# Optimization experiments

Hardware: AMD Instinct MI355X
Metric: run time of the kernel (lower is better)

Reference implementation:

```python
import jax, jax.numpy as jnp
import numpy as np

V, D, H, L, S = 50257, 1024, 16, 4, 4096
DH = D // H  # 64
DF = 4 * D   # 4096


def _layernorm(x, g, b, eps=1e-5):
    m = jnp.mean(x, axis=-1, keepdims=True)
    v = jnp.mean(jnp.square(x - m), axis=-1, keepdims=True)
    return (x - m) / jnp.sqrt(v + eps) * g + b


def _pos_encoding(s, d):
    # standard sinusoidal positional encoding [s, d]
    pos = jnp.arange(s, dtype=jnp.float32)[:, None]
    i = jnp.arange(d // 2, dtype=jnp.float32)[None, :]
    ang = pos * jnp.exp(-(2.0 * i / d) * jnp.log(10000.0))
    return jnp.concatenate([jnp.sin(ang), jnp.cos(ang)], axis=-1)


def setup_inputs() -> dict:
    key = jax.random.key(0)
    ks = jax.random.split(key, 8)
    s = 0.02
    return {
        "tokens": jax.random.randint(ks[0], (S,), 0, V),
        "emb": jax.random.normal(ks[1], (V, D), jnp.float32) * s,
        "Wq": jax.random.normal(ks[2], (L, H, D, DH), jnp.float32) * s,
        "bq": jnp.zeros((L, H, DH), jnp.float32),
        "Wk": jax.random.normal(ks[3], (L, H, D, DH), jnp.float32) * s,
        "bk": jnp.zeros((L, H, DH), jnp.float32),
        "Wv": jax.random.normal(ks[4], (L, H, D, DH), jnp.float32) * s,
        "bv": jnp.zeros((L, H, DH), jnp.float32),
        "ln1_g": jnp.ones((L, D), jnp.float32),
        "ln1_b": jnp.zeros((L, D), jnp.float32),
        "W1": jax.random.normal(ks[5], (L, D, DF), jnp.float32) * s,
        "b1": jnp.zeros((L, DF), jnp.float32),
        "W2": jax.random.normal(ks[6], (L, DF, D), jnp.float32) * s,
        "b2": jnp.zeros((L, D), jnp.float32),
        "ln2_g": jnp.ones((L, D), jnp.float32),
        "ln2_b": jnp.zeros((L, D), jnp.float32),
        "Wout": jax.random.normal(ks[7], (D, V), jnp.float32) * s,
        "bout": jnp.zeros((V,), jnp.float32),
    }


def reference(tokens, emb, Wq, bq, Wk, bk, Wv, bv, ln1_g, ln1_b,
              W1, b1, W2, b2, ln2_g, ln2_b, Wout, bout):
    x = emb[tokens] + _pos_encoding(S, D)          # [S, D]
    scale = 1.0 / jnp.sqrt(jnp.float32(DH))
    for l in range(L):
        # per-head projections: [H, S, DH]
        q = jnp.einsum("sd,hde->hse", x, Wq[l]) + bq[l][:, None, :]
        k = jnp.einsum("sd,hde->hse", x, Wk[l]) + bk[l][:, None, :]
        v = jnp.einsum("sd,hde->hse", x, Wv[l]) + bv[l][:, None, :]
        att = jax.nn.softmax(jnp.einsum("hse,hte->hst", q, k) * scale, axis=-1)
        y = jnp.einsum("hst,hte->hse", att, v)      # [H, S, DH]
        y = jnp.transpose(y, (1, 0, 2)).reshape(S, D)  # concat heads
        x = _layernorm(x + y, ln1_g[l], ln1_b[l])
        y = jnp.maximum(x @ W1[l] + b1[l], 0.0) @ W2[l] + b2[l]  # FFN
        x = _layernorm(x + y, ln2_g[l], ln2_b[l])
    logits = x @ Wout + bout                        # [S, V]
    return jax.nn.softmax(logits, axis=-1)
```

## Files before the change

kernel.cpp:

```cpp
#include <hip/hip_runtime.h>
#include <math.h>

#define S_LEN  4096
#define DMODEL 1024
#define NHEAD  16
#define DHEAD  64
#define DFF    4096
#define NLAYER 4
#define VOCAB  50257
#define NCBP   400

typedef unsigned short ushort_t;
typedef __attribute__((ext_vector_type(8))) __bf16 bf16x8;
typedef __attribute__((ext_vector_type(4))) float f32x4;

static __device__ __forceinline__ ushort_t f2bf(float f) {
  union { float f; unsigned u; } x; x.f = f;
  unsigned r = x.u + 0x7fffu + ((x.u >> 16) & 1u);
  return (ushort_t)(r >> 16);
}
static __device__ __forceinline__ float bf2f(ushort_t h) {
  union { unsigned u; float f; } x; x.u = ((unsigned)h) << 16;
  return x.f;
}
static __device__ __forceinline__ float exp2fast(float x) {
  return __builtin_amdgcn_exp2f(x);
}

#define GLOAD_LDS16(gp, lp) \
  __builtin_amdgcn_global_load_lds((const __attribute__((address_space(1))) void*)(gp), \
                                   (__attribute__((address_space(3))) void*)(lp), 16, 0, 0)

#define QSCALE 0.18033688011112042f

__global__ __launch_bounds__(256) void embed_kernel(
    const int* __restrict__ tokens, const float* __restrict__ emb,
    float* __restrict__ x, ushort_t* __restrict__ xh)
{
  int s = blockIdx.x;
  int tok = tokens[s];
  int d0 = threadIdx.x * 4;
  const double lf = 0.01798894603901598653;
  float4 ev = *(const float4*)(emb + (size_t)tok * DMODEL + d0);
  float o[4]; float evr[4] = {ev.x, ev.y, ev.z, ev.w};
  #pragma unroll
  for (int j = 0; j < 4; ++j) {
    int d = d0 + j;
    int i = (d < 512) ? d : d - 512;
    double ang = (double)s * exp(-lf * (double)i);
    float pe = (d < 512) ? (float)sin(ang) : (float)cos(ang);
    o[j] = evr[j] + pe;
  }
  *(float4*)(x + (size_t)s * DMODEL + d0) = make_float4(o[0], o[1], o[2], o[3]);
  ushort_t hv[4];
  #pragma unroll
  for (int j = 0; j < 4; ++j) hv[j] = f2bf(o[j]);
  *(ushort4*)(xh + (size_t)s * DMODEL + d0) = make_ushort4(hv[0], hv[1], hv[2], hv[3]);
}

__global__ __launch_bounds__(256)
void transpose_split(const float* __restrict__ in, ushort_t* __restrict__ oh,
                     ushort_t* __restrict__ ol,
                     long in_zstr, long out_zoff, long in_z2str, long out_z2off,
                     int zdiv, int in_rstride, int Kout, int Nvalid)
{
  __shared__ float tile[64][65];
  int z1 = blockIdx.z % zdiv, z2 = blockIdx.z / zdiv;
  long ioff = (long)z1 * in_zstr + (long)z2 * in_z2str;
  long ooff = (long)z1 * out_zoff + (long)z2 * out_z2off;
  const float* inz = in + ioff;
  ushort_t* ohz = oh + ooff;
  ushort_t* olz = ol + ooff;
  int k0 = blockIdx.x * 64, n0 = blockIdx.y * 64;
  int t = threadIdx.x;
  #pragma unroll
  for (int i = 0; i < 4; ++i) {
    int idx = t + i * 256;
    int kk = idx >> 4, c4 = idx & 15;
    #pragma unroll
    for (int j = 0; j < 4; ++j) {
      int n = n0 + c4 * 4 + j;
      float v = (n < Nvalid) ? inz[(long)(k0 + kk) * in_rstride + n] : 0.f;
      tile[c4 * 4 + j][kk] = v;
    }
  }
  __syncthreads();
  #pragma unroll
  for (int i = 0; i < 4; ++i) {
    int idx = t + i * 256;
    int nn = idx >> 4, k4 = idx & 15;
    ushort_t hv[4], lv[4];
    #pragma unroll
    for (int j = 0; j < 4; ++j) {
      float v = tile[nn][k4 * 4 + j];
      hv[j] = f2bf(v);
      lv[j] = f2bf(v - bf2f(hv[j]));
    }
    long ob = (long)(n0 + nn) * Kout + k0 + k4 * 4;
    *(ushort4*)(ohz + ob) = make_ushort4(hv[0], hv[1], hv[2], hv[3]);
    *(ushort4*)(olz + ob) = make_ushort4(lv[0], lv[1], lv[2], lv[3]);
  }
}

__global__ __launch_bounds__(256)
void transpose_h(const float* __restrict__ in, ushort_t* __restrict__ oh,
                 int in_rstride, int Kout, int Nvalid)
{
  __shared__ float tile[64][65];
  int k0 = blockIdx.x * 64, n0 = blockIdx.y * 64;
  int t = threadIdx.x;
  #pragma unroll
  for (int i = 0; i < 4; ++i) {
    int idx = t + i * 256;
    int kk = idx >> 4, c4 = idx & 15;
    #pragma unroll
    for (int j = 0; j < 4; ++j) {
      int n = n0 + c4 * 4 + j;
      float v = (n < Nvalid) ? in[(long)(k0 + kk) * in_rstride + n] : 0.f;
      tile[c4 * 4 + j][kk] = v;
    }
  }
  __syncthreads();
  #pragma unroll
  for (int i = 0; i < 4; ++i) {
    int idx = t + i * 256;
    int nn = idx >> 4, k4 = idx & 15;
    ushort_t hv[4];
    #pragma unroll
    for (int j = 0; j < 4; ++j) hv[j] = f2bf(tile[nn][k4 * 4 + j]);
    long ob = (long)(n0 + nn) * Kout + k0 + k4 * 4;
    *(ushort4*)(oh + ob) = make_ushort4(hv[0], hv[1], hv[2], hv[3]);
  }
}

__global__ __launch_bounds__(256)
void concat3_kernel(const float* __restrict__ a, const float* __restrict__ b,
                    const float* __restrict__ c, float* __restrict__ o,
                    int n, long lstrA, long lstrO)
{
  int i = blockIdx.x * 256 + threadIdx.x;
  long l = blockIdx.y;
  if (i < n) {
    o[l * lstrO + i]         = a[l * lstrA + i];
    o[l * lstrO + n + i]     = b[l * lstrA + i];
    o[l * lstrO + 2 * n + i] = c[l * lstrA + i];
  }
}

template<int EPI, bool RELU>
__global__ __launch_bounds__(512, 2)
void gemm8p(const ushort_t* __restrict__ Ah,
            const ushort_t* __restrict__ Bh, const ushort_t* __restrict__ Bl,
            const float* __restrict__ bias, float* __restrict__ C,
            ushort_t* __restrict__ O0, ushort_t* __restrict__ O1,
            ushort_t* __restrict__ O2, ushort_t* __restrict__ O4,
            int K, int ldk, long ldc, long czStride)
{
  constexpr int BUFSTR = 3 * 8192;
  constexpr int OBH = 8192, OBL = 16384;
  __shared__ ushort_t lds[2 * BUFSTR];

  const int t = threadIdx.x;
  const int l = t & 63;
  const int w = t >> 6;
  const int wr = w >> 2;
  const int wc = w & 3;
  const int lrow = l & 15;
  const int lk = (l >> 4) * 8;
  const int l8 = l * 8;
  const long m0 = (long)blockIdx.x * 256;
  const long n0 = (long)blockIdx.y * 256;
  const long kz = (long)blockIdx.z * K;

  const ushort_t *agp[2], *bgp[2], *blgp[2];
  int dst[2];
  #pragma unroll
  for (int i = 0; i < 2; ++i) {
    int s = i * 8 + w;
    dst[i] = s * 512 + l8;
    agp[i]  = Ah + (m0 + s * 16 + lrow) * (long)ldk + kz + lk;
    bgp[i]  = Bh + (n0 + s * 16 + lrow) * (long)ldk + kz + lk;
    blgp[i] = Bl + (n0 + s * 16 + lrow) * (long)ldk + kz + lk;
  }

  f32x4 acc[8][4];
  #pragma unroll
  for (int m = 0; m < 8; ++m)
    #pragma unroll
    for (int n = 0; n < 4; ++n) acc[m][n] = (f32x4)0.f;

  GLOAD_LDS16(agp[0],  &lds[dst[0]]);
  GLOAD_LDS16(agp[1],  &lds[dst[1]]);
  GLOAD_LDS16(bgp[0],  &lds[OBH + dst[0]]);
  GLOAD_LDS16(bgp[1],  &lds[OBH + dst[1]]);
  GLOAD_LDS16(blgp[0], &lds[OBL + dst[0]]);
  GLOAD_LDS16(blgp[1], &lds[OBL + dst[1]]);

  const int nk = K >> 5;
  int cur = 0;
  for (int kt = 0; kt < nk; ++kt) {
    const int knx = (kt + 1 < nk) ? (kt + 1) * 32 : 0;
    ushort_t* cb = &lds[cur * BUFSTR];
    ushort_t* nb = &lds[(cur ^ 1) * BUFSTR];
    bf16x8 af[8], bhf[4], blf[4];

    asm volatile("s_waitcnt vmcnt(2)" ::: "memory");
    __builtin_amdgcn_sched_barrier(0);
    __builtin_amdgcn_s_barrier();
    __builtin_amdgcn_sched_barrier(0);
    #pragma unroll
    for (int m = 0; m < 8; ++m)
      af[m] = *(const bf16x8*)&cb[(wr * 8 + m) * 512 + l8];
    #pragma unroll
    for (int n = 0; n < 4; ++n)
      bhf[n] = *(const bf16x8*)&cb[OBH + (wc * 4 + n) * 512 + l8];
    GLOAD_LDS16(agp[0] + knx, &nb[dst[0]]);
    GLOAD_LDS16(agp[1] + knx, &nb[dst[1]]);
    GLOAD_LDS16(bgp[0] + knx, &nb[OBH + dst[0]]);
    __builtin_amdgcn_s_setprio(1);
    #pragma unroll
    for (int m = 0; m < 8; ++m)
      #pragma unroll
      for (int n = 0; n < 4; ++n)
        acc[m][n] = __builtin_amdgcn_mfma_f32_16x16x32_bf16(af[m], bhf[n], acc[m][n], 0, 0, 0);
    __builtin_amdgcn_s_setprio(0);
    __builtin_amdgcn_sched_barrier(0);

    asm volatile("s_waitcnt vmcnt(3)" ::: "memory");
    __builtin_amdgcn_sched_barrier(0);
    __builtin_amdgcn_s_barrier();
    __builtin_amdgcn_sched_barrier(0);
    #pragma unroll
    for (int n = 0; n < 4; ++n)
      blf[n] = *(const bf16x8*)&cb[OBL + (wc * 4 + n) * 512 + l8];
    GLOAD_LDS16(bgp[1] + knx,  &nb[OBH + dst[1]]);
    GLOAD_LDS16(blgp[0] + knx, &nb[OBL + dst[0]]);
    GLOAD_LDS16(blgp[1] + knx, &nb[OBL + dst[1]]);
    __builtin_amdgcn_s_setprio(1);
    #pragma unroll
    for (int m = 0; m < 8; ++m)
      #pragma unroll
      for (int n = 0; n < 4; ++n)
        acc[m][n] = __builtin_amdgcn_mfma_f32_16x16x32_bf16(af[m], blf[n], acc[m][n], 0, 0, 0);
    __builtin_amdgcn_s_setprio(0);
    __builtin_amdgcn_sched_barrier(0);
    cur ^= 1;
  }
  asm volatile("s_waitcnt vmcnt(0)" ::: "memory");

  if constexpr (EPI == 2) {
    #pragma unroll
    for (int n = 0; n < 4; ++n) {
      long col = n0 + wc * 64 + n * 16 + lrow;
      float bv = bias[col];
      #pragma unroll
      for (int m = 0; m < 8; ++m) {
        #pragma unroll
        for (int r = 0; r < 4; ++r) {
          long row = m0 + wr * 128 + m * 16 + (l >> 4) * 4 + r;
          float v = acc[m][n][r] + bv;
          int c = (int)col;
          if (c < 1024) {
            int hh = c >> 6, e = c & 63;
            float qv = v * QSCALE;
            ushort_t hi = f2bf(qv);
            size_t a = ((size_t)hh * S_LEN + row) * 64 + e;
            O0[a] = hi; O1[a] = f2bf(qv - bf2f(hi));
          } else if (c < 2048) {
            int cc = c - 1024;
            int hh = cc >> 6, e = cc & 63;
            size_t a = ((size_t)hh * S_LEN + row) * 64 + e;
            O2[a] = f2bf(v);
          } else {
            int cc = c - 2048;
            int hh = cc >> 6, e = cc & 63;
            size_t a = ((size_t)hh * DHEAD + e) * S_LEN + row;
            O4[a] = f2bf(v);
          }
        }
      }
    }
  } else if constexpr (EPI == 1) {
    long col4[4]; float bv4[4];
    #pragma unroll
    for (int n = 0; n < 4; ++n) {
      col4[n] = n0 + wc * 64 + n * 16 + lrow;
      bv4[n] = bias[col4[n]];
    }
    #pragma unroll
    for (int m = 0; m < 8; ++m) {
      #pragma unroll
      for (int r = 0; r < 4; ++r) {
        long row = m0 + wr * 128 + m * 16 + (l >> 4) * 4 + r;
        ushort_t* crow = O0 + row * ldc;
        #pragma unroll
        for (int n = 0; n < 4; ++n) {
          float v = acc[m][n][r] + bv4[n];
          if (RELU) v = fmaxf(v, 0.f);
          crow[col4[n]] = f2bf(v);
        }
      }
    }
  } else {
    float* Cz = C + (long)blockIdx.z * czStride;
    long col4[4];
    #pragma unroll
    for (int n = 0; n < 4; ++n) col4[n] = n0 + wc * 64 + n * 16 + lrow;
    #pragma unroll
    for (int m = 0; m < 8; ++m) {
      #pragma unroll
      for (int r = 0; r < 4; ++r) {
        long row = m0 + wr * 128 + m * 16 + (l >> 4) * 4 + r;
        float* crow = Cz + row * ldc;
        #pragma unroll
        for (int n = 0; n < 4; ++n) crow[col4[n]] = acc[m][n][r];
      }
    }
  }
}

template<bool BOUND>
__global__ __launch_bounds__(512, 2)
void gemm1p(const ushort_t* __restrict__ Ah, const ushort_t* __restrict__ Bh,
            const float* __restrict__ bias, float* __restrict__ C,
            int K, int ldk, long ldc, int Nlimit,
            float* __restrict__ Ppart, int cbbase)
{
  constexpr int OB = 8192;
  constexpr int BUFSTR = 16384;
  __shared__ ushort_t lds[3 * BUFSTR];
  __shared__ float psum[1024];

  const int t = threadIdx.x;
  const int l = t & 63;
  const int w = t >> 6;
  const int wr = w >> 2;
  const int wc = w & 3;
  const int lrow = l & 15;
  const int lk = (l >> 4) * 8;
  const int l8 = l * 8;
  const long m0 = (long)blockIdx.x * 256;
  const long n0 = (long)blockIdx.y * 256;

  const ushort_t *agp[2], *bgp[2];
  int dst[2];
  #pragma unroll
  for (int i = 0; i < 2; ++i) {
    int s = i * 8 + w;
    dst[i] = s * 512 + l8;
    agp[i] = Ah + (m0 + s * 16 + lrow) * (long)ldk + lk;
    bgp[i] = Bh + (n0 + s * 16 + lrow) * (long)ldk + lk;
  }

  f32x4 acc[8][4];
  #pragma unroll
  for (int m = 0; m < 8; ++m)
    #pragma unroll
    for (int n = 0; n < 4; ++n) acc[m][n] = (f32x4)0.f;

  GLOAD_LDS16(agp[0], &lds[dst[0]]);
  GLOAD_LDS16(agp[1], &lds[dst[1]]);
  GLOAD_LDS16(bgp[0], &lds[OB + dst[0]]);
  GLOAD_LDS16(bgp[1], &lds[OB + dst[1]]);
  GLOAD_LDS16(agp[0] + 32, &lds[BUFSTR + dst[0]]);
  GLOAD_LDS16(agp[1] + 32, &lds[BUFSTR + dst[1]]);
  GLOAD_LDS16(bgp[0] + 32, &lds[BUFSTR + OB + dst[0]]);
  GLOAD_LDS16(bgp[1] + 32, &lds[BUFSTR + OB + dst[1]]);

  const int nk = K >> 5;
  int cur = 0;
  for (int kt = 0; kt < nk; ++kt) {
    ushort_t* cb = &lds[cur * BUFSTR];
    int nxt = cur + 2; if (nxt >= 3) nxt -= 3;
    ushort_t* nb = &lds[nxt * BUFSTR];
    bf16x8 af[8], bhf[4];

    asm volatile("s_waitcnt vmcnt(4)" ::: "memory");
    __builtin_amdgcn_sched_barrier(0);
    __builtin_amdgcn_s_barrier();
    __builtin_amdgcn_sched_barrier(0);
    #pragma unroll
    for (int m = 0; m < 8; ++m)
      af[m] = *(const bf16x8*)&cb[(wr * 8 + m) * 512 + l8];
    #pragma unroll
    for (int n = 0; n < 4; ++n)
      bhf[n] = *(const bf16x8*)&cb[OB + (wc * 4 + n) * 512 + l8];
    const int knx2 = (kt + 2 < nk) ? (kt + 2) * 32 : 0;
    GLOAD_LDS16(agp[0] + knx2, &nb[dst[0]]);
    GLOAD_LDS16(agp[1] + knx2, &nb[dst[1]]);
    GLOAD_LDS16(bgp[0] + knx2, &nb[OB + dst[0]]);
    GLOAD_LDS16(bgp[1] + knx2, &nb[OB + dst[1]]);
    __builtin_amdgcn_s_setprio(1);
    #pragma unroll
    for (int m = 0; m < 8; ++m)
      #pragma unroll
      for (int n = 0; n < 4; ++n)
        acc[m][n] = __builtin_amdgcn_mfma_f32_16x16x32_bf16(af[m], bhf[n], acc[m][n], 0, 0, 0);
    __builtin_amdgcn_s_setprio(0);
    __builtin_amdgcn_sched_barrier(0);
    cur = (cur == 2) ? 0 : cur + 1;
  }
  asm volatile("s_waitcnt vmcnt(0)" ::: "memory");

  float smr[8][4];
  #pragma unroll
  for (int m = 0; m < 8; ++m)
    #pragma unroll
    for (int r = 0; r < 4; ++r) smr[m][r] = 0.f;
  long col4[4]; float bv4[4]; bool cok4[4];
  #pragma unroll
  for (int n = 0; n < 4; ++n) {
    col4[n] = n0 + wc * 64 + n * 16 + lrow;
    cok4[n] = (!BOUND) || (col4[n] < (long)Nlimit);
    bv4[n] = cok4[n] ? bias[col4[n]] : 0.f;
  }
  #pragma unroll
  for (int m = 0; m < 8; ++m) {
    #pragma unroll
    for (int r = 0; r < 4; ++r) {
      long row = m0 + wr * 128 + m * 16 + (l >> 4) * 4 + r;
      float* crow = C + row * ldc;
      #pragma unroll
      for (int n = 0; n < 4; ++n) {
        float e = cok4[n] ? __expf(acc[m][n][r] + bv4[n]) : 0.f;
        if (cok4[n]) crow[col4[n]] = e;
        smr[m][r] += e;
      }
    }
  }
  #pragma unroll
  for (int m = 0; m < 8; ++m) {
    #pragma unroll
    for (int r = 0; r < 4; ++r) {
      float s = smr[m][r];
      s += __shfl_xor(s, 1);
      s += __shfl_xor(s, 2);
      s += __shfl_xor(s, 4);
      s += __shfl_xor(s, 8);
      if (lrow == 0)
        psum[wc * 256 + wr * 128 + m * 16 + (l >> 4) * 4 + r] = s;
    }
  }
  __syncthreads();
  if (t < 256) {
    float s = psum[t] + psum[256 + t] + psum[512 + t] + psum[768 + t];
    Ppart[(m0 + t) * NCBP + cbbase + blockIdx.y] = s;
  }
}

__global__ __launch_bounds__(256)
void attn_mfma(const ushort_t* __restrict__ qh, const ushort_t* __restrict__ ql,
               const ushort_t* __restrict__ kh, const ushort_t* __restrict__ vt,
               float* __restrict__ y)
{
  __shared__ ushort_t lds[24576];

  const int t = threadIdx.x, l = t & 63, w = t >> 6;
  const int lrow = l & 15, lhi = l >> 4;
  const int h = blockIdx.y;
  const int bw = blockIdx.x * 128 + w * 32;
  const size_t hS = (size_t)h * S_LEN * DHEAD;
  const size_t hV = (size_t)h * DHEAD * S_LEN;
  const int pb = 16384 + w * 2048;

  bf16x8 qhf[2][2], qlf[2][2];
  #pragma unroll
  for (int m = 0; m < 2; ++m)
    #pragma unroll
    for (int ks = 0; ks < 2; ++ks) {
      size_t a = hS + (size_t)(bw + m * 16 + lrow) * 64 + ks * 32 + lhi * 8;
      qhf[m][ks] = *(const bf16x8*)(qh + a);
      qlf[m][ks] = *(const bf16x8*)(ql + a);
    }

  f32x4 acc[2][4];
  #pragma unroll
  for (int m = 0; m < 2; ++m)
    #pragma unroll
    for (int n = 0; n < 4; ++n) acc[m][n] = (f32x4)0.f;
  float mrow[8], lsum[8];
  #pragma unroll
  for (int i = 0; i < 8; ++i) { mrow[i] = -1e30f; lsum[i] = 0.f; }

  #pragma unroll
  for (int i = 0; i < 2; ++i) {
    int s = i * 4 + w;
    size_t krow = (size_t)((s >> 1) * 16 + lrow);
    int koff = (s & 1) * 32 + lhi * 8;
    GLOAD_LDS16(kh + hS + krow * 64 + koff, &lds[s * 512 + l * 8]);
    int toff = (s & 1) * 32 + lhi * 8;
    GLOAD_LDS16(vt + hV + krow * S_LEN + toff, &lds[4096 + s * 512 + l * 8]);
  }

  int cur = 0;
  for (int kt = 0; kt < S_LEN; kt += 64) {
    asm volatile("s_waitcnt vmcnt(0)" ::: "memory");
    __builtin_amdgcn_sched_barrier(0);
    __builtin_amdgcn_s_barrier();
    __builtin_amdgcn_sched_barrier(0);
    ushort_t* cb = &lds[cur * 8192];
    if (kt + 64 < S_LEN) {
      ushort_t* nb = &lds[(cur ^ 1) * 8192];
      int kn = kt + 64;
      #pragma unroll
      for (int i = 0; i < 2; ++i) {
        int s = i * 4 + w;
        size_t krow = (size_t)(kn + (s >> 1) * 16 + lrow);
        int koff = (s & 1) * 32 + lhi * 8;
        GLOAD_LDS16(kh + hS + krow * 64 + koff, &nb[s * 512 + l * 8]);
        size_t erow = (size_t)((s >> 1) * 16 + lrow);
        int toff = kn + (s & 1) * 32 + lhi * 8;
        GLOAD_LDS16(vt + hV + erow * S_LEN + toff, &nb[4096 + s * 512 + l * 8]);
      }
    }

    f32x4 sacc[2][4];
    #pragma unroll
    for (int m = 0; m < 2; ++m)
      #pragma unroll
      for (int n = 0; n < 4; ++n) sacc[m][n] = (f32x4)0.f;
    #pragma unroll
    for (int ks = 0; ks < 2; ++ks) {
      bf16x8 bh_[4];
      #pragma unroll
      for (int n = 0; n < 4; ++n)
        bh_[n] = *(const bf16x8*)&cb[(n * 2 + ks) * 512 + l * 8];
      #pragma unroll
      for (int m = 0; m < 2; ++m)
        #pragma unroll
        for (int n = 0; n < 4; ++n) {
          sacc[m][n] = __builtin_amdgcn_mfma_f32_16x16x32_bf16(qhf[m][ks], bh_[n], sacc[m][n], 0, 0, 0);
          sacc[m][n] = __builtin_amdgcn_mfma_f32_16x16x32_bf16(qlf[m][ks], bh_[n], sacc[m][n], 0, 0, 0);
        }
    }

    float tmv[2][4];
    bool up = false;
    #pragma unroll
    for (int m = 0; m < 2; ++m) {
      #pragma unroll
      for (int r = 0; r < 4; ++r) {
        float tm = fmaxf(fmaxf(sacc[m][0][r], sacc[m][1][r]),
                         fmaxf(sacc[m][2][r], sacc[m][3][r]));
        tm = fmaxf(tm, __shfl_xor(tm, 1));
        tm = fmaxf(tm, __shfl_xor(tm, 2));
        tm = fmaxf(tm, __shfl_xor(tm, 4));
        tm = fmaxf(tm, __shfl_xor(tm, 8));
        tmv[m][r] = tm;
        up = up || (tm > mrow[m * 4 + r]);
      }
    }
    if (__ballot(up) != 0ULL) {
      #pragma unroll
      for (int m = 0; m < 2; ++m) {
        #pragma unroll
        for (int r = 0; r < 4; ++r) {
          const int idx = m * 4 + r;
          float mn = fmaxf(mrow[idx], tmv[m][r]);
          float al = exp2fast(mrow[idx] - mn);
          mrow[idx] = mn;
          lsum[idx] *= al;
          #pragma unroll
          for (int n = 0; n < 4; ++n) acc[m][n][r] *= al;
        }
      }
    }
    #pragma unroll
    for (int m = 0; m < 2; ++m) {
      #pragma unroll
      for (int r = 0; r < 4; ++r) {
        const int idx = m * 4 + r;
        float rs = 0.f;
        #pragma unroll
        for (int n = 0; n < 4; ++n) {
          float p = exp2fast(sacc[m][n][r] - mrow[idx]);
          rs += p;
          int pa = pb + ((m * 2 + (n >> 1)) << 9) + (((n & 1) * 2 + (lrow >> 3)) << 7)
                   + ((lhi * 4 + r) << 3) + (l & 7);
          pa ^= (lrow >> 3) << 3;
          lds[pa] = f2bf(p);
        }
        rs += __shfl_xor(rs, 1);
        rs += __shfl_xor(rs, 2);
        rs += __shfl_xor(rs, 4);
        rs += __shfl_xor(rs, 8);
        lsum[idx] += rs;
      }
    }

    #pragma unroll
    for (int ks = 0; ks < 2; ++ks) {
      bf16x8 pa_[2];
      #pragma unroll
      for (int m = 0; m < 2; ++m) {
        int ra = pb + ((m * 2 + ks) << 9) + (l << 3);
        ra ^= ((l >> 4) & 1) << 3;
        pa_[m] = *(const bf16x8*)&lds[ra];
      }
      #pragma unroll
      for (int n = 0; n < 4; ++n) {
        bf16x8 vf = *(const bf16x8*)&cb[4096 + (n * 2 + ks) * 512 + l * 8];
        #pragma unroll
        for (int m = 0; m < 2; ++m)
          acc[m][n] = __builtin_amdgcn_mfma_f32_16x16x32_bf16(pa_[m], vf, acc[m][n], 0, 0, 0);
      }
    }
    cur ^= 1;
  }

  #pragma unroll
  for (int m = 0; m < 2; ++m) {
    #pragma unroll
    for (int r = 0; r < 4; ++r) {
      float inv = 1.0f / lsum[m * 4 + r];
      int row = bw + m * 16 + lhi * 4 + r;
      #pragma unroll
      for (int n = 0; n < 4; ++n)
        y[(size_t)row * DMODEL + h * 64 + n * 16 + lrow] = acc[m][n][r] * inv;
    }
  }
}

__device__ __forceinline__ float block_sum256(float v, float* sm)
{
  #pragma unroll
  for (int off = 32; off >= 1; off >>= 1) v += __shfl_xor(v, off);
  int w = threadIdx.x >> 6;
  if ((threadIdx.x & 63) == 0) sm[w] = v;
  __syncthreads();
  v = sm[0] + sm[1] + sm[2] + sm[3];
  __syncthreads();
  return v;
}

__global__ __launch_bounds__(256)
void resid_ln_kernel(float* __restrict__ x, const float* __restrict__ y,
                     const float* __restrict__ g, const float* __restrict__ b,
                     ushort_t* __restrict__ xh)
{
  __shared__ float sm[4];
  int row = blockIdx.x, t = threadIdx.x;
  float4 xv = *(const float4*)(x + (size_t)row * DMODEL + t * 4);
  float4 yv = *(const float4*)(y + (size_t)row * DMODEL + t * 4);
  float a0 = xv.x + yv.x, a1 = xv.y + yv.y, a2 = xv.z + yv.z, a3 = xv.w + yv.w;
  float s = block_sum256(a0 + a1 + a2 + a3, sm);
  float mean = s * (1.0f / DMODEL);
  float d0 = a0 - mean, d1 = a1 - mean, d2 = a2 - mean, d3 = a3 - mean;
  float vs = block_sum256(d0*d0 + d1*d1 + d2*d2 + d3*d3, sm);
  float inv = rsqrtf(vs * (1.0f / DMODEL) + 1e-5f);
  float4 gv = *(const float4*)(g + t * 4);
  float4 bv = *(const float4*)(b + t * 4);
  float o[4];
  o[0] = d0 * inv * gv.x + bv.x;
  o[1] = d1 * inv * gv.y + bv.y;
  o[2] = d2 * inv * gv.z + bv.z;
  o[3] = d3 * inv * gv.w + bv.w;
  *(float4*)(x + (size_t)row * DMODEL + t * 4) = make_float4(o[0], o[1], o[2], o[3]);
  ushort_t hv[4];
  #pragma unroll
  for (int j = 0; j < 4; ++j) hv[j] = f2bf(o[j]);
  *(ushort4*)(xh + (size_t)row * DMODEL + t * 4) = make_ushort4(hv[0], hv[1], hv[2], hv[3]);
}

__global__ __launch_bounds__(256)
void resid_ln_red(float* __restrict__ x, const float* __restrict__ parts,
                  long pstride, const float* __restrict__ bias,
                  const float* __restrict__ g, const float* __restrict__ b,
                  ushort_t* __restrict__ xh)
{
  __shared__ float sm[4];
  int row = blockIdx.x, t = threadIdx.x;
  size_t base = (size_t)row * DMODEL + t * 4;
  float4 xv = *(const float4*)(x + base);
  float4 bb = *(const float4*)(bias + t * 4);
  float a0 = xv.x + bb.x, a1 = xv.y + bb.y, a2 = xv.z + bb.z, a3 = xv.w + bb.w;
  #pragma unroll
  for (int z = 0; z < 4; ++z) {
    float4 pv = *(const float4*)(parts + (size_t)z * pstride + base);
    a0 += pv.x; a1 += pv.y; a2 += pv.z; a3 += pv.w;
  }
  float s = block_sum256(a0 + a1 + a2 + a3, sm);
  float mean = s * (1.0f / DMODEL);
  float d0 = a0 - mean, d1 = a1 - mean, d2 = a2 - mean, d3 = a3 - mean;
  float vs = block_sum256(d0*d0 + d1*d1 + d2*d2 + d3*d3, sm);
  float inv = rsqrtf(vs * (1.0f / DMODEL) + 1e-5f);
  float4 gv = *(const float4*)(g + t * 4);
  float4 bv = *(const float4*)(b + t * 4);
  float o[4];
  o[0] = d0 * inv * gv.x + bv.x;
  o[1] = d1 * inv * gv.y + bv.y;
  o[2] = d2 * inv * gv.z + bv.z;
  o[3] = d3 * inv * gv.w + bv.w;
  *(float4*)(x + base) = make_float4(o[0], o[1], o[2], o[3]);
  ushort_t hv[4];
  #pragma unroll
  for (int j = 0; j < 4; ++j) hv[j] = f2bf(o[j]);
  *(ushort4*)(xh + base) = make_ushort4(hv[0], hv[1], hv[2], hv[3]);
}

__global__ __launch_bounds__(256)
void scale_softmax(float* __restrict__ out, const float* __restrict__ partials,
                   int ncb)
{
  __shared__ float sm[4];
  int row = blockIdx.x, t = threadIdx.x;
  float s = 0.f;
  for (int cb = t; cb < ncb; cb += 256) s += partials[(size_t)row * NCBP + cb];
  s = block_sum256(s, sm);
  float inv = 1.0f / s;
  float* p = out + (size_t)row * VOCAB;
  int head = (int)((((uintptr_t)16 - ((uintptr_t)p & 15)) & 15) >> 2);
  if (t < head) p[t] *= inv;
  int nvec = (VOCAB - head) >> 2;
  float4* pv = (float4*)(p + head);
  for (int i = t; i < nvec; i += 256) {
    float4 v = pv[i];
    v.x *= inv; v.y *= inv; v.z *= inv; v.w *= inv;
    pv[i] = v;
  }
  int done = head + nvec * 4;
  if (t < VOCAB - done) p[done + t] *= inv;
}

extern "C" void kernel_launch(void* const* d_in, const int* in_sizes, int n_in,
                              void* d_out, int out_size, void* d_ws, size_t ws_size,
                              hipStream_t stream)
{
  const int*   tokens = (const int*)  d_in[0];
  const float* emb    = (const float*)d_in[1];
  const float* Wq     = (const float*)d_in[2];
  const float* bq     = (const float*)d_in[3];
  const float* Wk     = (const float*)d_in[4];
  const float* bk     = (const float*)d_in[5];
  const float* Wv     = (const float*)d_in[6];
  const float* bv     = (const float*)d_in[7];
  const float* ln1g   = (const float*)d_in[8];
  const float* ln1b   = (const float*)d_in[9];
  const float* W1     = (const float*)d_in[10];
  const float* b1     = (const float*)d_in[11];
  const float* W2     = (const float*)d_in[12];
  const float* b2     = (const float*)d_in[13];
  const float* ln2g   = (const float*)d_in[14];
  const float* ln2b   = (const float*)d_in[15];
  const float* Wout   = (const float*)d_in[16];
  const float* bout   = (const float*)d_in[17];

  char* wsb = (char*)d_ws;
  ushort_t* xh     = (ushort_t*)(wsb);
  ushort_t* stripH = (ushort_t*)(wsb + ((size_t)8  << 20));
  float*    partials = (float*)(wsb + ((size_t)24 << 20));
  ushort_t* woutT  = (ushort_t*)(wsb + ((size_t)32 << 20));
  const bool bigws = ws_size >= ((size_t)137 << 20);

  char* ob = (char*)d_out;
  float*    x     = (float*)(ob);
  float*    yb    = (float*)(ob + ((size_t)16  << 20));
  ushort_t* qh    = (ushort_t*)(ob + ((size_t)32  << 20));
  ushort_t* ql    = (ushort_t*)(ob + ((size_t)40  << 20));
  ushort_t* kh    = (ushort_t*)(ob + ((size_t)48  << 20));
  ushort_t* vt    = (ushort_t*)(ob + ((size_t)56  << 20));
  ushort_t* h1h   = (ushort_t*)(ob + ((size_t)64  << 20));
  float*    fparts= (float*)(ob + ((size_t)96  << 20));
  ushort_t* wqkvhA= (ushort_t*)(ob + ((size_t)160 << 20));
  ushort_t* wqkvlA= (ushort_t*)(ob + ((size_t)184 << 20));
  ushort_t* w1hA  = (ushort_t*)(ob + ((size_t)208 << 20));
  ushort_t* w1lA  = (ushort_t*)(ob + ((size_t)240 << 20));
  ushort_t* w2hA  = (ushort_t*)(ob + ((size_t)272 << 20));
  ushort_t* w2lA  = (ushort_t*)(ob + ((size_t)304 << 20));
  float*    bqkvA = (float*)(ob + ((size_t)336 << 20));
  float*    outf  = (float*)d_out;

  const long WQKV_L = 3072L * 1024;
  const long WFF_L  = 4096L * 1024;

  embed_kernel<<<S_LEN, 256, 0, stream>>>(tokens, emb, x, xh);

  transpose_split<<<dim3(16, 1, 64), 256, 0, stream>>>(
      Wq, wqkvhA, wqkvlA,
      (long)DMODEL * DHEAD, (long)DHEAD * DMODEL,
      (long)NHEAD * DMODEL * DHEAD, WQKV_L,
      16, DHEAD, DMODEL, DHEAD);
  transpose_split<<<dim3(16, 1, 64), 256, 0, stream>>>(
      Wk, wqkvhA + 1024 * 1024, wqkvlA + 1024 * 1024,
      (long)DMODEL * DHEAD, (long)DHEAD * DMODEL,
      (long)NHEAD * DMODEL * DHEAD, WQKV_L,
      16, DHEAD, DMODEL, DHEAD);
  transpose_split<<<dim3(16, 1, 64), 256, 0, stream>>>(
      Wv, wqkvhA + 2048 * 1024, wqkvlA + 2048 * 1024,
      (long)DMODEL * DHEAD, (long)DHEAD * DMODEL,
      (long)NHEAD * DMODEL * DHEAD, WQKV_L,
      16, DHEAD, DMODEL, DHEAD);
  transpose_split<<<dim3(16, 64, 4), 256, 0, stream>>>(
      W1, w1hA, w1lA, 0, 0,
      (long)DMODEL * DFF, WFF_L, 1, DFF, DMODEL, DFF);
  transpose_split<<<dim3(64, 16, 4), 256, 0, stream>>>(
      W2, w2hA, w2lA, 0, 0,
      (long)DFF * DMODEL, WFF_L, 1, DMODEL, DFF, DMODEL);
  concat3_kernel<<<dim3(4, NLAYER), 256, 0, stream>>>(
      bq, bk, bv, bqkvA, 1024, 1024, 3072);

  for (int l = 0; l < NLAYER; ++l) {
    const ushort_t* wqh = wqkvhA + (long)l * WQKV_L;
    const ushort_t* wql = wqkvlA + (long)l * WQKV_L;
    const ushort_t* w1h = w1hA + (long)l * WFF_L;
    const ushort_t* w1l = w1lA + (long)l * WFF_L;
    const ushort_t* w2h = w2hA + (long)l * WFF_L;
    const ushort_t* w2l = w2lA + (long)l * WFF_L;

    gemm8p<2, false><<<dim3(16, 12), 512, 0, stream>>>(
        xh, wqh, wql, bqkvA + (long)l * 3072, nullptr,
        qh, ql, kh, vt, 1024, 1024, 0, 0);

    attn_mfma<<<dim3(32, 16), 256, 0, stream>>>(qh, ql, kh, vt, yb);

    resid_ln_kernel<<<S_LEN, 256, 0, stream>>>(x, yb,
        ln1g + (size_t)l * DMODEL, ln1b + (size_t)l * DMODEL, xh);

    gemm8p<1, true><<<dim3(16, 16), 512, 0, stream>>>(
        xh, w1h, w1l, b1 + (long)l * DFF, nullptr,
        h1h, nullptr, nullptr, nullptr, 1024, 1024, 4096, 0);
    gemm8p<0, false><<<dim3(16, 4, 4), 512, 0, stream>>>(
        h1h, w2h, w2l, nullptr, fparts,
        nullptr, nullptr, nullptr, nullptr,
        1024, 4096, 1024, (long)S_LEN * DMODEL);
    resid_ln_red<<<S_LEN, 256, 0, stream>>>(x, fparts, (long)S_LEN * DMODEL,
        b2 + (long)l * DMODEL,
        ln2g + (size_t)l * DMODEL, ln2b + (size_t)l * DMODEL, xh);
  }

  if (bigws) {
    transpose_h<<<dim3(16, 786, 1), 256, 0, stream>>>(
        Wout, woutT, VOCAB, DMODEL, VOCAB);
    gemm1p<true><<<dim3(16, 197), 512, 0, stream>>>(
        xh, woutT, bout, outf, 1024, 1024, VOCAB, VOCAB, partials, 0);
  } else {
    const int SW = 4096;
    for (int is = 0; is < 12; ++is) {
      int n0 = is * SW;
      transpose_h<<<dim3(16, 64, 1), 256, 0, stream>>>(
          Wout + n0, stripH, VOCAB, DMODEL, SW);
      gemm1p<false><<<dim3(16, 16), 512, 0, stream>>>(
          xh, stripH, bout + n0, outf + n0,
          1024, 1024, VOCAB, SW, partials, is * 16);
    }
    int n0 = 12 * SW;
    int ncols = VOCAB - n0;
    int nt64 = (ncols + 63) / 64;
    int nb256 = (ncols + 255) / 256;
    transpose_h<<<dim3(16, nt64, 1), 256, 0, stream>>>(
        Wout + n0, stripH, VOCAB, DMODEL, ncols);
    gemm1p<true><<<dim3(16, nb256), 512, 0, stream>>>(
        xh, stripH, bout + n0, outf + n0,
        1024, 1024, VOCAB, ncols, partials, 12 * 16);
  }
  const int ncb = (VOCAB + 255) / 256;
  scale_softmax<<<S_LEN, 256, 0, stream>>>(outf, partials, ncb);
}
```

Baseline: 3.214 ms.

## Deepen gemm1p LDS pipeline to four stages and add XCD-aware block swizzle

The output-projection GEMM (gemm1p) goes from a 3-buffer to a 4-buffer LDS ring. This keeps three K-tiles of global-to-LDS loads in flight, with the vmcnt wait raised to match, to better hide memory latency. Both GEMM kernels also remap their linear block index so that blocks landing on the same XCD cover neighbouring tiles, meant to improve L2 reuse of A and B. The partial-sum index now uses the remapped column. The cost is more LDS per block (about 132KB) and a small amount of index arithmetic.

```diff
diff --git a/kernel.cpp b/kernel.cpp
--- a/kernel.cpp
+++ b/kernel.cpp
@@ -25,6 +25,17 @@
 }
 static __device__ __forceinline__ float exp2fast(float x) {
   return __builtin_amdgcn_exp2f(x);
+}
+
+static __device__ __forceinline__ void xcd_swizzle(int& bx, int& by) {
+  int gx = gridDim.x;
+  int nwg = gx * gridDim.y;
+  int lin = blockIdx.y * gx + blockIdx.x;
+  if ((nwg & 7) == 0) {
+    int cpx = nwg >> 3;
+    int s = (lin & 7) * cpx + (lin >> 3);
+    bx = s % gx; by = s / gx;
+  } else { bx = blockIdx.x; by = blockIdx.y; }
 }
 
 #define GLOAD_LDS16(gp, lp) \
@@ -168,8 +179,10 @@
   const int lrow = l & 15;
   const int lk = (l >> 4) * 8;
   const int l8 = l * 8;
-  const long m0 = (long)blockIdx.x * 256;
-  const long n0 = (long)blockIdx.y * 256;
+  int bxs, bys;
+  xcd_swizzle(bxs, bys);
+  const long m0 = (long)bxs * 256;
+  const long n0 = (long)bys * 256;
   const long kz = (long)blockIdx.z * K;
 
   const ushort_t *agp[2], *bgp[2], *blgp[2];
@@ -328,7 +341,7 @@
 {
   constexpr int OB = 8192;
   constexpr int BUFSTR = 16384;
-  __shared__ ushort_t lds[3 * BUFSTR];
+  __shared__ ushort_t lds[4 * BUFSTR];
   __shared__ float psum[1024];
 
   const int t = threadIdx.x;
@@ -339,8 +352,10 @@
   const int lrow = l & 15;
   const int lk = (l >> 4) * 8;
   const int l8 = l * 8;
-  const long m0 = (long)blockIdx.x * 256;
-  const long n0 = (long)blockIdx.y * 256;
+  int bxs, bys;
+  xcd_swizzle(bxs, bys);
+  const long m0 = (long)bxs * 256;
+  const long n0 = (long)bys * 256;
 
   const ushort_t *agp[2], *bgp[2];
   int dst[2];
@@ -358,24 +373,22 @@
     #pragma unroll
     for (int n = 0; n < 4; ++n) acc[m][n] = (f32x4)0.f;
 
-  GLOAD_LDS16(agp[0], &lds[dst[0]]);
-  GLOAD_LDS16(agp[1], &lds[dst[1]]);
-  GLOAD_LDS16(bgp[0], &lds[OB + dst[0]]);
-  GLOAD_LDS16(bgp[1], &lds[OB + dst[1]]);
-  GLOAD_LDS16(agp[0] + 32, &lds[BUFSTR + dst[0]]);
-  GLOAD_LDS16(agp[1] + 32, &lds[BUFSTR + dst[1]]);
-  GLOAD_LDS16(bgp[0] + 32, &lds[BUFSTR + OB + dst[0]]);
-  GLOAD_LDS16(bgp[1] + 32, &lds[BUFSTR + OB + dst[1]]);
+  #pragma unroll
+  for (int tt = 0; tt < 3; ++tt) {
+    GLOAD_LDS16(agp[0] + tt * 32, &lds[tt * BUFSTR + dst[0]]);
+    GLOAD_LDS16(agp[1] + tt * 32, &lds[tt * BUFSTR + dst[1]]);
+    GLOAD_LDS16(bgp[0] + tt * 32, &lds[tt * BUFSTR + OB + dst[0]]);
+    GLOAD_LDS16(bgp[1] + tt * 32, &lds[tt * BUFSTR + OB + dst[1]]);
+  }
 
   const int nk = K >> 5;
   int cur = 0;
   for (int kt = 0; kt < nk; ++kt) {
     ushort_t* cb = &lds[cur * BUFSTR];
-    int nxt = cur + 2; if (nxt >= 3) nxt -= 3;
-    ushort_t* nb = &lds[nxt * BUFSTR];
+    ushort_t* nb = &lds[((cur + 3) & 3) * BUFSTR];
     bf16x8 af[8], bhf[4];
 
-    asm volatile("s_waitcnt vmcnt(4)" ::: "memory");
+    asm volatile("s_waitcnt vmcnt(8)" ::: "memory");
     __builtin_amdgcn_sched_barrier(0);
     __builtin_amdgcn_s_barrier();
     __builtin_amdgcn_sched_barrier(0);
@@ -385,11 +398,11 @@
     #pragma unroll
     for (int n = 0; n < 4; ++n)
       bhf[n] = *(const bf16x8*)&cb[OB + (wc * 4 + n) * 512 + l8];
-    const int knx2 = (kt + 2 < nk) ? (kt + 2) * 32 : 0;
-    GLOAD_LDS16(agp[0] + knx2, &nb[dst[0]]);
-    GLOAD_LDS16(agp[1] + knx2, &nb[dst[1]]);
-    GLOAD_LDS16(bgp[0] + knx2, &nb[OB + dst[0]]);
-    GLOAD_LDS16(bgp[1] + knx2, &nb[OB + dst[1]]);
+    const int knx3 = (kt + 3 < nk) ? (kt + 3) * 32 : 0;
+    GLOAD_LDS16(agp[0] + knx3, &nb[dst[0]]);
+    GLOAD_LDS16(agp[1] + knx3, &nb[dst[1]]);
+    GLOAD_LDS16(bgp[0] + knx3, &nb[OB + dst[0]]);
+    GLOAD_LDS16(bgp[1] + knx3, &nb[OB + dst[1]]);
     __builtin_amdgcn_s_setprio(1);
     #pragma unroll
     for (int m = 0; m < 8; ++m)
@@ -398,7 +411,7 @@
         acc[m][n] = __builtin_amdgcn_mfma_f32_16x16x32_bf16(af[m], bhf[n], acc[m][n], 0, 0, 0);
     __builtin_amdgcn_s_setprio(0);
     __builtin_amdgcn_sched_barrier(0);
-    cur = (cur == 2) ? 0 : cur + 1;
+    cur = (cur + 1) & 3;
   }
   asm volatile("s_waitcnt vmcnt(0)" ::: "memory");
 
@@ -444,7 +457,7 @@
   __syncthreads();
   if (t < 256) {
     float s = psum[t] + psum[256 + t] + psum[512 + t] + psum[768 + t];
-    Ppart[(m0 + t) * NCBP + cbbase + blockIdx.y] = s;
+    Ppart[(m0 + t) * NCBP + cbbase + bys] = s;
   }
 }
 
```

Result: slower. 3.279 ms (+2.0%).
